# Kernel optimization log

Hardware: AMD Instinct MI355X
Metric: run time of the kernel (lower is better)

The kernel has to match this reference:

```python
import jax, jax.numpy as jnp
import numpy as np

N = 100000
E = 1600000
D_IN = 128
H = 128
OUT = 10
NUM_LAYERS = 3
G = 512  # number of graphs


def setup_inputs() -> dict:
    key = jax.random.key(0)
    ks = jax.random.split(key, 20)
    x = jax.random.normal(ks[0], (N, D_IN), dtype=jnp.float32)
    edge_index = jax.random.randint(ks[1], (2, E), 0, N, dtype=jnp.int64)
    batch = jnp.sort(jax.random.randint(ks[2], (N,), 0, G, dtype=jnp.int64))
    s = 1.0 / np.sqrt(H)
    inp = {"x": x, "edge_index": edge_index, "batch": batch}
    # GCN layer weights (layer 0: D_IN->H, layers 1,2: H->H)
    inp["W0"] = jax.random.normal(ks[3], (D_IN, H), dtype=jnp.float32) * s
    inp["b0"] = jnp.zeros((H,), jnp.float32)
    inp["W1"] = jax.random.normal(ks[4], (H, H), dtype=jnp.float32) * s
    inp["b1"] = jnp.zeros((H,), jnp.float32)
    inp["W2"] = jax.random.normal(ks[5], (H, H), dtype=jnp.float32) * s
    inp["b2"] = jnp.zeros((H,), jnp.float32)
    # gate_nn: Linear(H,H) -> ReLU -> Linear(H,1)
    inp["gW1"] = jax.random.normal(ks[6], (H, H), dtype=jnp.float32) * s
    inp["gb1"] = jnp.zeros((H,), jnp.float32)
    inp["gW2"] = jax.random.normal(ks[7], (H, 1), dtype=jnp.float32) * s
    inp["gb2"] = jnp.zeros((1,), jnp.float32)
    # MLP head: Linear(H,H) -> ReLU -> Dropout -> Linear(H,OUT)
    inp["lW1"] = jax.random.normal(ks[8], (H, H), dtype=jnp.float32) * s
    inp["lb1"] = jnp.zeros((H,), jnp.float32)
    inp["lW2"] = jax.random.normal(ks[9], (H, OUT), dtype=jnp.float32) * s
    inp["lb2"] = jnp.zeros((OUT,), jnp.float32)
    return inp


def _gcn_norm(edge_index):
    # add self-loops, then symmetric normalization (PyG gcn_norm, fill_value=1)
    loops = jnp.arange(N, dtype=edge_index.dtype)
    row = jnp.concatenate([edge_index[0], loops])
    col = jnp.concatenate([edge_index[1], loops])
    deg = jax.ops.segment_sum(jnp.ones_like(col, dtype=jnp.float32), col, num_segments=N)
    dis = jnp.where(deg > 0, jax.lax.rsqrt(jnp.maximum(deg, 1e-12)), 0.0)
    return row, col, dis[row] * dis[col]


def _gcn_layer(x, W, b, row, col, norm):
    h = x @ W                                   # [N,H]
    msg = norm[:, None] * h[row]                # gather + scale, [E+N,H]
    agg = jax.ops.segment_sum(msg, col, num_segments=N)
    return agg + b


def _segment_softmax(gate, batch):
    # gate: [N], batch: [N] sorted graph ids
    gmax = jax.ops.segment_max(gate, batch, num_segments=G)
    e = jnp.exp(gate - gmax[batch])
    denom = jax.ops.segment_sum(e, batch, num_segments=G)
    return e / denom[batch]


def reference(x, edge_index, batch, W0, b0, W1, b1, W2, b2,
              gW1, gb1, gW2, gb2, lW1, lb1, lW2, lb2):
    row, col, norm = _gcn_norm(edge_index)
    # stacked GCN layers with ReLU (dropout is identity at inference)
    h = jax.nn.relu(_gcn_layer(x, W0, b0, row, col, norm))
    h = jax.nn.relu(_gcn_layer(h, W1, b1, row, col, norm))
    h = jax.nn.relu(_gcn_layer(h, W2, b2, row, col, norm))
    # GlobalAttention pooling: gate_nn -> segment softmax -> weighted sum
    gate = (jax.nn.relu(h @ gW1 + gb1) @ gW2 + gb2)[:, 0]  # [N]
    a = _segment_softmax(gate, batch)                       # [N]
    pooled = jax.ops.segment_sum(a[:, None] * h, batch, num_segments=G)  # [G,H]
    # MLP head
    logits = jax.nn.relu(pooled @ lW1 + lb1) @ lW2 + lb2    # [G,OUT]
    return logits, jnp.zeros((), dtype=x.dtype)
```

## Files before the change

### kernel.cpp

```cpp
#include <hip/hip_runtime.h>
#include <math.h>

#define NN 100000
#define EE 1600000
#define HH 128
#define GG 512
#define OUTD 10
#define NB 196
#define BSH 9

typedef _Float16 f16x2 __attribute__((ext_vector_type(2)));
typedef _Float16 f16x4 __attribute__((ext_vector_type(4)));
typedef _Float16 f16x8 __attribute__((ext_vector_type(8)));
typedef float f32x4 __attribute__((ext_vector_type(4)));

__global__ void init_kernel(int* gs, int* ge, int* bcount, float* out) {
  int i = blockIdx.x * 256 + threadIdx.x;
  if (i < GG) { gs[i] = 0; ge[i] = 0; }
  if (i < NB) bcount[i] = 0;
  if (i == 0) out[GG * OUTD] = 0.0f;
}

__global__ __launch_bounds__(256) void binA_kernel(const int* __restrict__ ei,
                                                   int* __restrict__ bcount) {
  __shared__ int lh[NB];
  for (int i = threadIdx.x; i < NB; i += 256) lh[i] = 0;
  __syncthreads();
  int e = blockIdx.x * 2048 + threadIdx.x;
#pragma unroll
  for (int i = 0; i < 8; i++, e += 256)
    if (e < EE) atomicAdd(&lh[ei[EE + e] >> BSH], 1);
  __syncthreads();
  for (int i = threadIdx.x; i < NB; i += 256)
    if (lh[i]) atomicAdd(&bcount[i], lh[i]);
}

__global__ __launch_bounds__(256) void bscan_kernel(const int* __restrict__ bcount,
                                                    int* __restrict__ boffs,
                                                    int* __restrict__ bcursor) {
  __shared__ int ts[256];
  int t = threadIdx.x;
  int v = (t < NB) ? bcount[t] : 0;
  ts[t] = v;
  __syncthreads();
  for (int off = 1; off < 256; off <<= 1) {
    int x = (t >= off) ? ts[t - off] : 0;
    __syncthreads();
    ts[t] += x;
    __syncthreads();
  }
  int excl = (t == 0) ? 0 : ts[t - 1];
  if (t < NB) { boffs[t] = excl; bcursor[t] = excl; }
  if (t == NB - 1) boffs[NB] = excl + v;
}

__global__ __launch_bounds__(256) void binB_kernel(const int* __restrict__ ei,
                                                   int* __restrict__ bcursor,
                                                   int2* __restrict__ ebuf) {
  __shared__ int lh[NB];
  __shared__ int lbase[NB];
  for (int i = threadIdx.x; i < NB; i += 256) lh[i] = 0;
  __syncthreads();
  int e0 = blockIdx.x * 2048 + threadIdx.x;
  int r_[8], c_[8], rank_[8];
  int e = e0;
#pragma unroll
  for (int i = 0; i < 8; i++, e += 256) {
    if (e < EE) {
      r_[i] = ei[e];
      c_[i] = ei[EE + e];
      rank_[i] = atomicAdd(&lh[c_[i] >> BSH], 1);
    }
  }
  __syncthreads();
  for (int i = threadIdx.x; i < NB; i += 256)
    lbase[i] = lh[i] ? atomicAdd(&bcursor[i], lh[i]) : 0;
  __syncthreads();
  e = e0;
#pragma unroll
  for (int i = 0; i < 8; i++, e += 256) {
    if (e < EE) {
      int b = c_[i] >> BSH;
      ebuf[lbase[b] + rank_[i]] = make_int2(r_[i], c_[i]);
    }
  }
}

__global__ __launch_bounds__(256) void binD_kernel(const int2* __restrict__ ebuf,
                                                   const int* __restrict__ boffs,
                                                   int* __restrict__ deg) {
  __shared__ int lcnt[512];
  int b = blockIdx.x;
  for (int i = threadIdx.x; i < 512; i += 256) lcnt[i] = 0;
  __syncthreads();
  int s = boffs[b], e = boffs[b + 1];
  for (int i = s + threadIdx.x; i < e; i += 256)
    atomicAdd(&lcnt[ebuf[i].y & 511], 1);
  __syncthreads();
  int base = b << BSH;
  for (int i = threadIdx.x; i < 512; i += 256) {
    int node = base + i;
    if (node < NN) deg[node] = lcnt[i] + 1;
  }
}

__global__ __launch_bounds__(256) void scan1_kernel(const int* __restrict__ deg,
                                                    int* __restrict__ offs,
                                                    int* __restrict__ bsums) {
  __shared__ int ts[256];
  int t = threadIdx.x;
  int base = blockIdx.x * 2048 + t * 8;
  int v[8]; int s = 0;
#pragma unroll
  for (int i = 0; i < 8; i++) {
    int idx = base + i;
    int c = (idx < NN) ? (deg[idx] - 1) : 0;
    v[i] = s; s += c;
  }
  ts[t] = s;
  __syncthreads();
  for (int off = 1; off < 256; off <<= 1) {
    int x = (t >= off) ? ts[t - off] : 0;
    __syncthreads();
    ts[t] += x;
    __syncthreads();
  }
  int excl = (t == 0) ? 0 : ts[t - 1];
  if (t == 255) bsums[blockIdx.x] = ts[255];
#pragma unroll
  for (int i = 0; i < 8; i++) {
    int idx = base + i;
    if (idx < NN) offs[idx] = excl + v[i];
  }
}

__global__ void scan2_kernel(int* bsums, int nb) {
  if (threadIdx.x == 0 && blockIdx.x == 0) {
    int s = 0;
    for (int b = 0; b < nb; b++) { int x = bsums[b]; bsums[b] = s; s += x; }
  }
}

__global__ void scan3_kernel(const int* __restrict__ deg, int* __restrict__ offs,
                             float* __restrict__ dis, const int* __restrict__ bsums) {
  int i = blockIdx.x * 256 + threadIdx.x;
  if (i >= NN) return;
  int o = offs[i] + bsums[i >> 11];
  offs[i] = o;
  dis[i] = rsqrtf((float)deg[i]);
  if (i == NN - 1) offs[NN] = EE;
}

__global__ __launch_bounds__(256) void binC_kernel(const int2* __restrict__ ebuf,
                                                   const int* __restrict__ boffs,
                                                   const int* __restrict__ offs,
                                                   const float* __restrict__ dis,
                                                   int2* __restrict__ csr_p) {
  __shared__ int lcur[512];
  int b = blockIdx.x;
  int base = b << BSH;
  for (int i = threadIdx.x; i < 512; i += 256) {
    int node = base + i;
    lcur[i] = (node < NN) ? offs[node] : 0;
  }
  __syncthreads();
  int s = boffs[b], e = boffs[b + 1];
  for (int i = s + threadIdx.x; i < e; i += 256) {
    int2 rc = ebuf[i];
    int slot = atomicAdd(&lcur[rc.y & 511], 1);
    csr_p[slot] = make_int2(rc.x, __float_as_int(dis[rc.x]));
  }
}

__global__ void prep_kernel(const float* __restrict__ W0, const float* __restrict__ W1,
                            const float* __restrict__ W2, const float* __restrict__ gW1,
                            _Float16* __restrict__ Wt) {
  int idx = blockIdx.x * 256 + threadIdx.x;
  int m = idx >> 14;
  int rem = idx & 16383;
  int c = rem >> 7;
  int k = rem & 127;
  const float* src = (m == 0) ? W0 : (m == 1) ? W1 : (m == 2) ? W2 : gW1;
  Wt[idx] = (_Float16)src[k * 128 + c];
}

template <int AF32, int MODE>
__global__ __launch_bounds__(256) void gemm_kernel(const void* __restrict__ Av,
                                                   const _Float16* __restrict__ Wt,
                                                   const float* __restrict__ bias,
                                                   _Float16* __restrict__ out,
                                                   const float* __restrict__ gW2,
                                                   const float* __restrict__ gb2,
                                                   float* __restrict__ gate, int nrows) {
  __shared__ __align__(16) _Float16 wlds[128 * 136];
  int t = threadIdx.x;
  const uint4* src = (const uint4*)Wt;
#pragma unroll
  for (int i = 0; i < 8; i++) {
    int q = t + 256 * i;
    int c = q >> 4, p = q & 15;
    *(uint4*)&wlds[c * 136 + p * 8] = src[q];
  }
  __syncthreads();

  int wid = t >> 6, l = t & 63;
  int wr0 = blockIdx.x * 64 + wid * 16;
  int row = wr0 + (l & 15);
  bool valid = row < nrows;
  f16x8 zero8 = {(_Float16)0, (_Float16)0, (_Float16)0, (_Float16)0,
                 (_Float16)0, (_Float16)0, (_Float16)0, (_Float16)0};
  f16x8 af[4];
  if (AF32) {
    const float* ap = (const float*)Av + (size_t)row * 128;
#pragma unroll
    for (int kt = 0; kt < 4; kt++) {
      if (valid) {
        const float4* p4 = (const float4*)(ap + kt * 32 + (l >> 4) * 8);
        float4 u0 = p4[0], u1 = p4[1];
        f16x8 a;
        a[0] = (_Float16)u0.x; a[1] = (_Float16)u0.y; a[2] = (_Float16)u0.z; a[3] = (_Float16)u0.w;
        a[4] = (_Float16)u1.x; a[5] = (_Float16)u1.y; a[6] = (_Float16)u1.z; a[7] = (_Float16)u1.w;
        af[kt] = a;
      } else af[kt] = zero8;
    }
  } else {
    const _Float16* ap = (const _Float16*)Av + (size_t)row * 128;
#pragma unroll
    for (int kt = 0; kt < 4; kt++)
      af[kt] = valid ? *(const f16x8*)(ap + kt * 32 + (l >> 4) * 8) : zero8;
  }

  f32x4 acc[8] = {};
  int ko = (l >> 4) * 16;
#pragma unroll
  for (int n = 0; n < 8; n++) {
    int col = n * 16 + (l & 15);
    const char* base = (const char*)wlds + col * 272;
#pragma unroll
    for (int kt = 0; kt < 4; kt++) {
      f16x8 b = *(const f16x8*)(base + kt * 64 + ko);
      acc[n] = __builtin_amdgcn_mfma_f32_16x16x32_f16(af[kt], b, acc[n], 0, 0, 0);
    }
  }

  if (MODE == 0) {
#pragma unroll
    for (int n = 0; n < 8; n++) {
      int col = n * 16 + (l & 15);
#pragma unroll
      for (int r = 0; r < 4; r++) {
        int orow = wr0 + (l >> 4) * 4 + r;
        if (orow < nrows) out[(size_t)orow * 128 + col] = (_Float16)acc[n][r];
      }
    }
  } else {
    float gp[4] = {0.f, 0.f, 0.f, 0.f};
    int c = l & 15;
#pragma unroll
    for (int n = 0; n < 8; n++) {
      int col = n * 16 + c;
      float bv = bias[col];
      float wv = gW2[col];
#pragma unroll
      for (int r = 0; r < 4; r++) gp[r] += fmaxf(acc[n][r] + bv, 0.f) * wv;
    }
#pragma unroll
    for (int m = 1; m < 16; m <<= 1) {
#pragma unroll
      for (int r = 0; r < 4; r++) gp[r] += __shfl_xor(gp[r], m);
    }
    if (c == 0) {
      float gb = gb2[0];
#pragma unroll
      for (int r = 0; r < 4; r++) {
        int orow = wr0 + (l >> 4) * 4 + r;
        if (orow < nrows) gate[orow] = gp[r] + gb;
      }
    }
  }
}

__global__ __launch_bounds__(256) void agg_kernel(const _Float16* __restrict__ t,
                                                  const int* __restrict__ offs,
                                                  const int2* __restrict__ csr_p,
                                                  const float* __restrict__ dis,
                                                  const float* __restrict__ bias,
                                                  _Float16* __restrict__ out) {
  int c = blockIdx.x * 4 + (threadIdx.x >> 6);
  if (c >= NN) return;
  int lane = threadIdx.x & 63;
  int half = lane >> 5;
  int cl = lane & 31;
  float dc = dis[c];
  int s = offs[c], e = offs[c + 1];
  const f16x4* t4 = (const f16x4*)t;

  float a0 = 0.f, a1 = 0.f, a2 = 0.f, a3 = 0.f;
  if (half == 0) {
    f16x4 hv = t4[(size_t)c * 32 + cl];
    a0 = dc * (float)hv[0]; a1 = dc * (float)hv[1];
    a2 = dc * (float)hv[2]; a3 = dc * (float)hv[3];
  }

  for (int k0 = s; k0 < e; k0 += 64) {
    int cnt = e - k0; if (cnt > 64) cnt = 64;
    int2 pe = csr_p[k0 + (lane < cnt ? lane : cnt - 1)];
    int j = 0;
    for (; j + 8 <= cnt; j += 8) {
      int i0 = j + half, i1 = j + 2 + half, i2 = j + 4 + half, i3 = j + 6 + half;
      int r0 = __shfl(pe.x, i0), r1 = __shfl(pe.x, i1);
      int r2 = __shfl(pe.x, i2), r3 = __shfl(pe.x, i3);
      float w0 = __int_as_float(__shfl(pe.y, i0));
      float w1 = __int_as_float(__shfl(pe.y, i1));
      float w2 = __int_as_float(__shfl(pe.y, i2));
      float w3 = __int_as_float(__shfl(pe.y, i3));
      f16x4 v0 = t4[(size_t)r0 * 32 + cl];
      f16x4 v1 = t4[(size_t)r1 * 32 + cl];
      f16x4 v2 = t4[(size_t)r2 * 32 + cl];
      f16x4 v3 = t4[(size_t)r3 * 32 + cl];
      a0 += w0 * (float)v0[0] + w1 * (float)v1[0] + w2 * (float)v2[0] + w3 * (float)v3[0];
      a1 += w0 * (float)v0[1] + w1 * (float)v1[1] + w2 * (float)v2[1] + w3 * (float)v3[1];
      a2 += w0 * (float)v0[2] + w1 * (float)v1[2] + w2 * (float)v2[2] + w3 * (float)v3[2];
      a3 += w0 * (float)v0[3] + w1 * (float)v1[3] + w2 * (float)v2[3] + w3 * (float)v3[3];
    }
    for (; j < cnt; j += 2) {
      int js = j + half;
      bool act = js < cnt;
      int jc = act ? js : cnt - 1;
      int r = __shfl(pe.x, jc);
      float w = act ? __int_as_float(__shfl(pe.y, jc)) : 0.f;
      f16x4 v = t4[(size_t)r * 32 + cl];
      a0 += w * (float)v[0]; a1 += w * (float)v[1];
      a2 += w * (float)v[2]; a3 += w * (float)v[3];
    }
  }

  a0 += __shfl_xor(a0, 32); a1 += __shfl_xor(a1, 32);
  a2 += __shfl_xor(a2, 32); a3 += __shfl_xor(a3, 32);

  if (half == 0) {
    const float4 bv = *(const float4*)&bias[4 * cl];
    f16x4 o;
    o[0] = (_Float16)fmaxf(a0 * dc + bv.x, 0.f);
    o[1] = (_Float16)fmaxf(a1 * dc + bv.y, 0.f);
    o[2] = (_Float16)fmaxf(a2 * dc + bv.z, 0.f);
    o[3] = (_Float16)fmaxf(a3 * dc + bv.w, 0.f);
    ((f16x4*)out)[(size_t)c * 32 + cl] = o;
  }
}

__global__ void bounds_kernel(const int* __restrict__ batch, int* gs, int* ge) {
  int i = blockIdx.x * 256 + threadIdx.x;
  if (i >= NN) return;
  int b = batch[i];
  if (i == 0 || batch[i - 1] != b) gs[b] = i;
  if (i == NN - 1 || batch[i + 1] != b) ge[b] = i + 1;
}

__global__ __launch_bounds__(256) void poolhead_kernel(
    const _Float16* __restrict__ h, const float* __restrict__ gate,
    const int* __restrict__ gs, const int* __restrict__ ge,
    const float* __restrict__ lW1, const float* __restrict__ lb1,
    const float* __restrict__ lW2, const float* __restrict__ lb2,
    float* __restrict__ out) {
  int g = blockIdx.x;
  int t = threadIdx.x;
  int s = gs[g], e = ge[g];
  __shared__ float red[4];
  __shared__ float pax[4][64], pay[4][64];
  __shared__ float pooled[128];
  __shared__ float hid[128];
  int wid = t >> 6, lane = t & 63;

  float m = -3.0e38f;
  for (int i = s + t; i < e; i += 256) m = fmaxf(m, gate[i]);
#pragma unroll
  for (int o = 32; o > 0; o >>= 1) m = fmaxf(m, __shfl_xor(m, o));
  if (lane == 0) red[wid] = m;
  __syncthreads();
  m = fmaxf(fmaxf(red[0], red[1]), fmaxf(red[2], red[3]));
  __syncthreads();

  float ds_ = 0.f;
  for (int i = s + t; i < e; i += 256) ds_ += __expf(gate[i] - m);
#pragma unroll
  for (int o = 32; o > 0; o >>= 1) ds_ += __shfl_xor(ds_, o);
  if (lane == 0) red[wid] = ds_;
  __syncthreads();
  float denom = red[0] + red[1] + red[2] + red[3];

  const f16x2* h2 = (const f16x2*)h;
  int cp = t & 63, q = t >> 6;
  float px = 0.f, py = 0.f;
  for (int i = s + q; i < e; i += 4) {
    float w = __expf(gate[i] - m);
    f16x2 v = h2[(size_t)i * 64 + cp];
    px += w * (float)v[0];
    py += w * (float)v[1];
  }
  pax[q][cp] = px; pay[q][cp] = py;
  __syncthreads();
  if (t < 64) {
    float inv = (e > s) ? 1.f / denom : 0.f;
    float sx = pax[0][t] + pax[1][t] + pax[2][t] + pax[3][t];
    float sy = pay[0][t] + pay[1][t] + pay[2][t] + pay[3][t];
    pooled[2 * t] = sx * inv;
    pooled[2 * t + 1] = sy * inv;
  }
  __syncthreads();

  if (t < 128) {
    float hv = lb1[t];
    for (int k = 0; k < 128; k++) hv += pooled[k] * lW1[k * 128 + t];
    hid[t] = fmaxf(hv, 0.f);
  }
  __syncthreads();

  if (t < OUTD) {
    float acc2 = lb2[t];
    for (int k = 0; k < 128; k++) acc2 += hid[k] * lW2[k * OUTD + t];
    out[g * OUTD + t] = acc2;
  }
}

extern "C" void kernel_launch(void* const* d_in, const int* in_sizes, int n_in,
                              void* d_out, int out_size, void* d_ws, size_t ws_size,
                              hipStream_t stream) {
  const float* x   = (const float*)d_in[0];
  const int*   ei  = (const int*)d_in[1];
  const int* batch = (const int*)d_in[2];
  const float* W0  = (const float*)d_in[3];
  const float* b0  = (const float*)d_in[4];
  const float* W1  = (const float*)d_in[5];
  const float* b1  = (const float*)d_in[6];
  const float* W2  = (const float*)d_in[7];
  const float* b2  = (const float*)d_in[8];
  const float* gW1 = (const float*)d_in[9];
  const float* gb1 = (const float*)d_in[10];
  const float* gW2 = (const float*)d_in[11];
  const float* gb2 = (const float*)d_in[12];
  const float* lW1 = (const float*)d_in[13];
  const float* lb1 = (const float*)d_in[14];
  const float* lW2 = (const float*)d_in[15];
  const float* lb2 = (const float*)d_in[16];
  float* out = (float*)d_out;

  char* w = (char*)d_ws;
  auto alloc = [&](size_t bytes) {
    char* p = w;
    w += (bytes + 255) & ~(size_t)255;
    return p;
  };
  _Float16* T  = (_Float16*)alloc((size_t)NN * 128 * 2);
  _Float16* HA = (_Float16*)alloc((size_t)NN * 128 * 2);
  _Float16* HB = (_Float16*)alloc((size_t)NN * 128 * 2);
  _Float16* Wt = (_Float16*)alloc((size_t)4 * 128 * 128 * 2);
  int* deg     = (int*)alloc((size_t)NN * 4);
  int* offs    = (int*)alloc((size_t)(NN + 1) * 4);
  float* dis   = (float*)alloc((size_t)NN * 4);
  int2* csr_p  = (int2*)alloc((size_t)EE * 8);
  int2* ebuf   = (int2*)alloc((size_t)EE * 8);
  float* gate  = (float*)alloc((size_t)NN * 4);
  int* bsums   = (int*)alloc(64 * 4);
  int* gs      = (int*)alloc(GG * 4);
  int* ge      = (int*)alloc(GG * 4);
  int* bcount  = (int*)alloc(NB * 4);
  int* boffs   = (int*)alloc((NB + 1) * 4);
  int* bcursor = (int*)alloc(NB * 4);

  dim3 b256(256);
  init_kernel<<<dim3(2), b256, 0, stream>>>(gs, ge, bcount, out);
  prep_kernel<<<dim3(256), b256, 0, stream>>>(W0, W1, W2, gW1, Wt);
  binA_kernel<<<dim3((EE + 2047) / 2048), b256, 0, stream>>>(ei, bcount);
  bscan_kernel<<<dim3(1), b256, 0, stream>>>(bcount, boffs, bcursor);
  binB_kernel<<<dim3((EE + 2047) / 2048), b256, 0, stream>>>(ei, bcursor, ebuf);
  binD_kernel<<<dim3(NB), b256, 0, stream>>>(ebuf, boffs, deg);
  scan1_kernel<<<dim3(49), b256, 0, stream>>>(deg, offs, bsums);
  scan2_kernel<<<dim3(1), dim3(64), 0, stream>>>(bsums, 49);
  scan3_kernel<<<dim3((NN + 255) / 256), b256, 0, stream>>>(deg, offs, dis, bsums);
  binC_kernel<<<dim3(NB), b256, 0, stream>>>(ebuf, boffs, offs, dis, csr_p);

  int gblocks = (NN + 63) / 64;
  int ablocks = (NN + 3) / 4;
  gemm_kernel<1, 0><<<dim3(gblocks), b256, 0, stream>>>(x, Wt + 0 * 16384, nullptr, T, nullptr, nullptr, nullptr, NN);
  agg_kernel<<<dim3(ablocks), b256, 0, stream>>>(T, offs, csr_p, dis, b0, HA);
  gemm_kernel<0, 0><<<dim3(gblocks), b256, 0, stream>>>(HA, Wt + 1 * 16384, nullptr, T, nullptr, nullptr, nullptr, NN);
  agg_kernel<<<dim3(ablocks), b256, 0, stream>>>(T, offs, csr_p, dis, b1, HB);
  gemm_kernel<0, 0><<<dim3(gblocks), b256, 0, stream>>>(HB, Wt + 2 * 16384, nullptr, T, nullptr, nullptr, nullptr, NN);
  agg_kernel<<<dim3(ablocks), b256, 0, stream>>>(T, offs, csr_p, dis, b2, HA);

  gemm_kernel<0, 2><<<dim3(gblocks), b256, 0, stream>>>(HA, Wt + 3 * 16384, gb1, nullptr, gW2, gb2, gate, NN);
  bounds_kernel<<<dim3((NN + 255) / 256), b256, 0, stream>>>(batch, gs, ge);
  poolhead_kernel<<<dim3(GG), b256, 0, stream>>>(HA, gate, gs, ge, lW1, lb1, lW2, lb2, out);
}
```

Measured before the change: 474.7 us.

## Derive CSR offsets from bin offsets inside binD, dropping global scan kernels

Edges are already bucketed by destination-node bin, so each bin's global start offset is known from boffs. The per-node degree histogram in binD is now scanned in shared memory and added to the bin start to write CSR offsets and inverse-sqrt degrees directly. This removes the deg array and the three-kernel global scan (scan1/scan2/scan3), including a single-threaded serial scan, at the cost of a small in-block scan per bin.

```diff
diff --git a/kernel.cpp b/kernel.cpp
--- a/kernel.cpp
+++ b/kernel.cpp
@@ -88,67 +88,32 @@
 
 __global__ __launch_bounds__(256) void binD_kernel(const int2* __restrict__ ebuf,
                                                    const int* __restrict__ boffs,
-                                                   int* __restrict__ deg) {
+                                                   int* __restrict__ offs,
+                                                   float* __restrict__ dis) {
   __shared__ int lcnt[512];
-  int b = blockIdx.x;
-  for (int i = threadIdx.x; i < 512; i += 256) lcnt[i] = 0;
+  __shared__ int lsum[256];
+  int b = blockIdx.x, t = threadIdx.x;
+  for (int i = t; i < 512; i += 256) lcnt[i] = 0;
   __syncthreads();
   int s = boffs[b], e = boffs[b + 1];
-  for (int i = s + threadIdx.x; i < e; i += 256)
+  for (int i = s + t; i < e; i += 256)
     atomicAdd(&lcnt[ebuf[i].y & 511], 1);
   __syncthreads();
+  int c0 = lcnt[2 * t], c1 = lcnt[2 * t + 1];
+  lsum[t] = c0 + c1;
+  __syncthreads();
+  for (int off = 1; off < 256; off <<= 1) {
+    int x = (t >= off) ? lsum[t - off] : 0;
+    __syncthreads();
+    lsum[t] += x;
+    __syncthreads();
+  }
+  int excl = (t == 0) ? 0 : lsum[t - 1];
   int base = b << BSH;
-  for (int i = threadIdx.x; i < 512; i += 256) {
-    int node = base + i;
-    if (node < NN) deg[node] = lcnt[i] + 1;
-  }
-}
-
-__global__ __launch_bounds__(256) void scan1_kernel(const int* __restrict__ deg,
-                                                    int* __restrict__ offs,
-                                                    int* __restrict__ bsums) {
-  __shared__ int ts[256];
-  int t = threadIdx.x;
-  int base = blockIdx.x * 2048 + t * 8;
-  int v[8]; int s = 0;
-#pragma unroll
-  for (int i = 0; i < 8; i++) {
-    int idx = base + i;
-    int c = (idx < NN) ? (deg[idx] - 1) : 0;
-    v[i] = s; s += c;
-  }
-  ts[t] = s;
-  __syncthreads();
-  for (int off = 1; off < 256; off <<= 1) {
-    int x = (t >= off) ? ts[t - off] : 0;
-    __syncthreads();
-    ts[t] += x;
-    __syncthreads();
-  }
-  int excl = (t == 0) ? 0 : ts[t - 1];
-  if (t == 255) bsums[blockIdx.x] = ts[255];
-#pragma unroll
-  for (int i = 0; i < 8; i++) {
-    int idx = base + i;
-    if (idx < NN) offs[idx] = excl + v[i];
-  }
-}
-
-__global__ void scan2_kernel(int* bsums, int nb) {
-  if (threadIdx.x == 0 && blockIdx.x == 0) {
-    int s = 0;
-    for (int b = 0; b < nb; b++) { int x = bsums[b]; bsums[b] = s; s += x; }
-  }
-}
-
-__global__ void scan3_kernel(const int* __restrict__ deg, int* __restrict__ offs,
-                             float* __restrict__ dis, const int* __restrict__ bsums) {
-  int i = blockIdx.x * 256 + threadIdx.x;
-  if (i >= NN) return;
-  int o = offs[i] + bsums[i >> 11];
-  offs[i] = o;
-  dis[i] = rsqrtf((float)deg[i]);
-  if (i == NN - 1) offs[NN] = EE;
+  int n0 = base + 2 * t, n1 = base + 2 * t + 1;
+  if (n0 < NN) { offs[n0] = s + excl;      dis[n0] = rsqrtf((float)(c0 + 1)); }
+  if (n1 < NN) { offs[n1] = s + excl + c0; dis[n1] = rsqrtf((float)(c1 + 1)); }
+  if (b == 0 && t == 0) offs[NN] = EE;
 }
 
 __global__ __launch_bounds__(256) void binC_kernel(const int2* __restrict__ ebuf,
@@ -455,13 +420,11 @@
   _Float16* HA = (_Float16*)alloc((size_t)NN * 128 * 2);
   _Float16* HB = (_Float16*)alloc((size_t)NN * 128 * 2);
   _Float16* Wt = (_Float16*)alloc((size_t)4 * 128 * 128 * 2);
-  int* deg     = (int*)alloc((size_t)NN * 4);
   int* offs    = (int*)alloc((size_t)(NN + 1) * 4);
   float* dis   = (float*)alloc((size_t)NN * 4);
   int2* csr_p  = (int2*)alloc((size_t)EE * 8);
   int2* ebuf   = (int2*)alloc((size_t)EE * 8);
   float* gate  = (float*)alloc((size_t)NN * 4);
-  int* bsums   = (int*)alloc(64 * 4);
   int* gs      = (int*)alloc(GG * 4);
   int* ge      = (int*)alloc(GG * 4);
   int* bcount  = (int*)alloc(NB * 4);
@@ -474,10 +437,7 @@
   binA_kernel<<<dim3((EE + 2047) / 2048), b256, 0, stream>>>(ei, bcount);
   bscan_kernel<<<dim3(1), b256, 0, stream>>>(bcount, boffs, bcursor);
   binB_kernel<<<dim3((EE + 2047) / 2048), b256, 0, stream>>>(ei, bcursor, ebuf);
-  binD_kernel<<<dim3(NB), b256, 0, stream>>>(ebuf, boffs, deg);
-  scan1_kernel<<<dim3(49), b256, 0, stream>>>(deg, offs, bsums);
-  scan2_kernel<<<dim3(1), dim3(64), 0, stream>>>(bsums, 49);
-  scan3_kernel<<<dim3((NN + 255) / 256), b256, 0, stream>>>(deg, offs, dis, bsums);
+  binD_kernel<<<dim3(NB), b256, 0, stream>>>(ebuf, boffs, offs, dis);
   binC_kernel<<<dim3(NB), b256, 0, stream>>>(ebuf, boffs, offs, dis, csr_p);
 
   int gblocks = (NN + 63) / 64;
```

New measurement: 459.7 us. -3.2%, faster.
